# Kernel tuning notes

Hardware: AMD Instinct MI355X
Metric: run time of the kernel (lower is better)

Reference implementation:

```python
import jax, jax.numpy as jnp
import numpy as np

# Config (decoder-only Transformer)
NL, H, D, DK, V, B, S = 6, 16, 1024, 64, 32000, 2, 1024  # DK = d_v = D // H
DFF = 4 * D


def _layer_norm(x, g, b, eps=1e-5):
    mu = jnp.mean(x, axis=-1, keepdims=True)
    var = jnp.mean(jnp.square(x - mu), axis=-1, keepdims=True)
    return (x - mu) * jax.lax.rsqrt(var + eps) * g + b


def _pos_encoding(seq_len, d_embed):
    # Matches PositionalEncoding: base 1000 (as in source), sin at even i, cos at odd i
    pos = jnp.arange(seq_len, dtype=jnp.float32)[:, None]
    i = jnp.arange(d_embed, dtype=jnp.float32)[None, :]
    angle = pos / jnp.power(1000.0, i / d_embed)
    return jnp.where((jnp.arange(d_embed)[None, :] % 2) == 0, jnp.sin(angle), jnp.cos(angle))


def setup_inputs() -> dict:
    key = jax.random.key(0)
    ks = jax.random.split(key, 8)
    n = lambda k, shp, sc: jax.random.normal(k, shp, dtype=jnp.float32) * sc
    return {
        "outputs": jax.random.randint(ks[0], (B, S), 0, V),
        "embed": n(ks[1], (V, D), 0.02),
        # per-head Q/K/V projections stacked over layers and heads: [NL, H, D, DK]
        "Wq": n(ks[2], (NL, H, D, DK), D ** -0.5),
        "Wk": n(ks[3], (NL, H, D, DK), D ** -0.5),
        "Wv": n(ks[4], (NL, H, D, DK), D ** -0.5),
        "W1": n(ks[5], (NL, D, DFF), D ** -0.5),
        "W2": n(ks[6], (NL, DFF, D), DFF ** -0.5),
        "ln1_g": jnp.ones((NL, D), jnp.float32),
        "ln1_b": jnp.zeros((NL, D), jnp.float32),
        "ln2_g": jnp.ones((NL, D), jnp.float32),
        "ln2_b": jnp.zeros((NL, D), jnp.float32),
        "Wout": n(ks[7], (D, V), D ** -0.5),
        "bout": jnp.zeros((V,), jnp.float32),
    }


def reference(outputs, embed, Wq, Wk, Wv, W1, W2, ln1_g, ln1_b, ln2_g, ln2_b, Wout, bout):
    x = embed[outputs]                      # [B, S, D]
    x = x + _pos_encoding(S, D)
    scale = jnp.float32(DK ** 0.5)
    for l in range(NL):
        # Masked multi-head self-attention (per-head projections batched over H)
        q = jnp.einsum('bsd,hdk->bhsk', x, Wq[l])
        k = jnp.einsum('bsd,hdk->bhsk', x, Wk[l])
        v = jnp.einsum('bsd,hdk->bhsk', x, Wv[l])
        scores = jnp.einsum('bhqk,bhsk->bhqs', q, k) / scale   # [B,H,S,S]
        # Faithful to source: tril then masked_fill(score == 0, -inf)
        scores = jnp.tril(scores)
        scores = jnp.where(scores == 0, -jnp.inf, scores)
        w = jax.nn.softmax(scores, axis=-1)
        attn = jnp.einsum('bhqs,bhsv->bqhv', w, v).reshape(B, S, H * DK)
        x = _layer_norm(x + attn, ln1_g[l], ln1_b[l])
        # Position-wise FFN (dropout is identity at inference)
        h = jax.nn.relu(x @ W1[l]) @ W2[l]
        x = _layer_norm(x + h, ln2_g[l], ln2_b[l])
    return x @ Wout + bout                  # logits [B, S, V]
```

## Files before the change

kernel.cpp:

```cpp
#include <hip/hip_runtime.h>

typedef unsigned short u16;
typedef __attribute__((ext_vector_type(8))) short short8;
typedef __attribute__((ext_vector_type(4))) short short4_t;
typedef __attribute__((ext_vector_type(4))) float f32x4;

#define NLAYER 6
#define NH 16
#define DMODEL 1024
#define DHEAD 64
#define NVOCAB 32000
#define NB 2
#define NS 1024
#define NDFF 4096
#define MTOK (NB*NS)

__device__ __forceinline__ u16 f2b(float f) {
    union { float f; unsigned u; } x; x.f = f;
    unsigned r = x.u + 0x7fffu + ((x.u >> 16) & 1u);
    return (u16)(r >> 16);
}

#define GLL16(gp, lp) __builtin_amdgcn_global_load_lds( \
    (const __attribute__((address_space(1))) void*)(gp), \
    (__attribute__((address_space(3))) void*)(lp), 16, 0, 0)

__global__ __launch_bounds__(256) void trans64(
    const float* __restrict__ src, u16* __restrict__ dst,
    int R, int C, long sStride, long dStride)
{
    __shared__ float sh[64][65];
    const int c0 = blockIdx.x * 64, r0 = blockIdx.y * 64;
    const float* s = src + (long)blockIdx.z * sStride;
    u16* d = dst + (long)blockIdx.z * dStride;
    const int tid = threadIdx.x;
    const int lr = tid >> 4, lc = (tid & 15) * 4;
    #pragma unroll
    for (int q = 0; q < 4; ++q) {
        const float4 v = *(const float4*)(s + (long)(r0 + q * 16 + lr) * C + c0 + lc);
        sh[q * 16 + lr][lc + 0] = v.x;
        sh[q * 16 + lr][lc + 1] = v.y;
        sh[q * 16 + lr][lc + 2] = v.z;
        sh[q * 16 + lr][lc + 3] = v.w;
    }
    __syncthreads();
    #pragma unroll
    for (int k = 0; k < 2; ++k) {
        const int t = tid + 256 * k;
        const int col = t >> 3, rch = (t & 7) * 8;
        u16 tmp[8];
        #pragma unroll
        for (int j = 0; j < 8; ++j) tmp[j] = f2b(sh[rch + j][col]);
        *(short8*)(d + (long)(c0 + col) * R + r0 + rch) = *(const short8*)tmp;
    }
}

__global__ void transpose_qkv(const float* __restrict__ src, u16* __restrict__ dst, int sel)
{
    __shared__ float t[32][33];
    const int bi = blockIdx.z, l = bi >> 4, h = bi & 15;
    const float* s = src + (long)bi * (DMODEL * DHEAD);
    u16* d = dst + (long)l * 3072 * DMODEL + (long)(sel * 1024 + h * 64) * DMODEL;
    const int c0 = blockIdx.x * 32, r0 = blockIdx.y * 32;
    const int tx = threadIdx.x, ty = threadIdx.y;
    #pragma unroll
    for (int j = 0; j < 32; j += 8)
        t[ty + j][tx] = s[(long)(r0 + ty + j) * DHEAD + c0 + tx];
    __syncthreads();
    #pragma unroll
    for (int j = 0; j < 32; j += 8)
        d[(long)(c0 + ty + j) * DMODEL + r0 + tx] = f2b(t[tx][ty + j]);
}

__global__ void embed_pe(const int* __restrict__ toks, const float* __restrict__ emb,
                         float* __restrict__ x, u16* __restrict__ xb)
{
    const int row = blockIdx.x;
    const int s = row & (NS - 1);
    const long erow = (long)toks[row] * DMODEL;
    const long base = (long)row * DMODEL;
    #pragma unroll
    for (int j = 0; j < 4; ++j) {
        int d = threadIdx.x + j * 256;
        float ang = (float)s * exp2f(-(float)d * (9.965784284662087f / 1024.f));
        float pe = (d & 1) ? cosf(ang) : sinf(ang);
        float v = emb[erow + d] + pe;
        x[base + d] = v;
        xb[base + d] = f2b(v);
    }
}

template<int ND>
__global__ __launch_bounds__(256) void ln_residual(
    const float* __restrict__ xin, const float* __restrict__ delta, size_t pstride,
    const float* __restrict__ g, const float* __restrict__ bb,
    float* __restrict__ xout, u16* __restrict__ xbout)
{
    __shared__ float red[8];
    const long base = (long)blockIdx.x * DMODEL;
    const int d = threadIdx.x * 4;
    f32x4 v = *(const f32x4*)(xin + base + d);
    #pragma unroll
    for (int y = 0; y < ND; ++y)
        v += *(const f32x4*)(delta + base + (size_t)y * pstride + d);
    float sum = v[0] + v[1] + v[2] + v[3];
    float sq  = v[0]*v[0] + v[1]*v[1] + v[2]*v[2] + v[3]*v[3];
    #pragma unroll
    for (int off = 1; off < 64; off <<= 1) {
        sum += __shfl_xor(sum, off, 64);
        sq  += __shfl_xor(sq,  off, 64);
    }
    const int wv = threadIdx.x >> 6, lane = threadIdx.x & 63;
    if (lane == 0) { red[wv] = sum; red[4 + wv] = sq; }
    __syncthreads();
    float ts = red[0] + red[1] + red[2] + red[3];
    float tq = red[4] + red[5] + red[6] + red[7];
    float mu = ts * (1.f / DMODEL);
    float var = tq * (1.f / DMODEL) - mu * mu;
    float rstd = rsqrtf(var + 1e-5f);
    const f32x4 gg = *(const f32x4*)(g + d);
    const f32x4 bv = *(const f32x4*)(bb + d);
    f32x4 yv = (v - mu) * rstd * gg + bv;
    *(f32x4*)(xout + base + d) = yv;
    u16 fourv[4];
    #pragma unroll
    for (int i = 0; i < 4; ++i) fourv[i] = f2b(yv[i]);
    *(short4_t*)(xbout + base + d) = *(const short4_t*)fourv;
}

template<int BM, int EPI>
__global__ __launch_bounds__(BM*2, 2) void gemm_pipe(
    const u16* __restrict__ A, const u16* __restrict__ Bt,
    void* __restrict__ Cout, const float* __restrict__ bias,
    int M, int N, int K, int lda, int ldb, size_t zstride)
{
    constexpr int WAVES = BM / 32;
    constexpr int WC = WAVES / 2;
    constexpr int MR = BM / 32;
    constexpr int TILE = BM * 32;

    __shared__ __align__(16) u16 As[4][TILE];
    __shared__ __align__(16) u16 Bs[4][TILE];

    const int nmb = M / BM;
    const int id = blockIdx.x, nwg = gridDim.x;
    const int q = nwg >> 3, r = nwg & 7, xcd = id & 7, loc = id >> 3;
    const int swz = (xcd < r ? xcd * (q + 1) : r * (q + 1) + (xcd - r) * q) + loc;
    const int m0 = (swz % nmb) * BM, n0 = (swz / nmb) * BM;
    const int koff = blockIdx.y * K;

    const int tid = threadIdx.x, wv = tid >> 6, lane = tid & 63;
    const int wr = wv / WC, wc = wv % WC;
    const int lrow = lane & 15, ks = lane >> 4;

    const u16* gsrc[4];
    int ldso[2];
    {
        const int l4 = lane >> 2, s = lane & 3;
        #pragma unroll
        for (int j = 0; j < 2; ++j) {
            const int row = j * (WAVES * 16) + wv * 16 + l4;
            const int x = (row >> 1) & 3;
            gsrc[j]     = A  + (size_t)(m0 + row) * lda + koff + (size_t)((s ^ x) * 8);
            gsrc[2 + j] = Bt + (size_t)(n0 + row) * ldb + koff + (size_t)((s ^ x) * 8);
            ldso[j] = (j * (WAVES * 16) + wv * 16) * 32;
        }
    }
    int aoff[MR], boff[4];
    #pragma unroll
    for (int m = 0; m < MR; ++m) {
        const int row = wr * (BM / 2) + m * 16 + lrow;
        aoff[m] = row * 32 + ((ks ^ ((row >> 1) & 3)) * 8);
    }
    #pragma unroll
    for (int n = 0; n < 4; ++n) {
        const int row = wc * 64 + n * 16 + lrow;
        boff[n] = row * 32 + ((ks ^ ((row >> 1) & 3)) * 8);
    }

    const int NT = K / 32;
    auto ISSUE = [&](int t) {
        const int b = t & 3;
        const size_t ko = (size_t)t * 32;
        #pragma unroll
        for (int j = 0; j < 2; ++j) {
            GLL16(gsrc[j] + ko,     &As[b][ldso[j]]);
            GLL16(gsrc[2 + j] + ko, &Bs[b][ldso[j]]);
        }
    };

    f32x4 acc[MR][4] = {};
    ISSUE(0); ISSUE(1); ISSUE(2);

    for (int t = 0; t < NT; ++t) {
        if (t < NT - 2)       { asm volatile("s_waitcnt vmcnt(8)" ::: "memory"); }
        else if (t == NT - 2) { asm volatile("s_waitcnt vmcnt(4)" ::: "memory"); }
        else                  { asm volatile("s_waitcnt vmcnt(0)" ::: "memory"); }
        __builtin_amdgcn_sched_barrier(0);
        __builtin_amdgcn_s_barrier();
        __builtin_amdgcn_sched_barrier(0);

        const int b = t & 3;
        short8 af[MR], bf[4];
        #pragma unroll
        for (int m = 0; m < MR; ++m) af[m] = *(const short8*)(&As[b][aoff[m]]);
        #pragma unroll
        for (int n = 0; n < 4; ++n)  bf[n] = *(const short8*)(&Bs[b][boff[n]]);
        if (t + 3 < NT) ISSUE(t + 3);
        __builtin_amdgcn_s_setprio(1);
        #pragma unroll
        for (int m = 0; m < MR; ++m)
            #pragma unroll
            for (int n = 0; n < 4; ++n)
                acc[m][n] = __builtin_amdgcn_mfma_f32_16x16x32_bf16(af[m], bf[n], acc[m][n], 0, 0, 0);
        __builtin_amdgcn_s_setprio(0);
    }

    if (EPI == 0 || EPI == 3) {
        __syncthreads();
        float* patch = (float*)((WAVES == 8 && (wv & 4)) ? (void*)&Bs[0][0] : (void*)&As[0][0])
                       + (wv & 3) * (16 * 68);
        const int cc0 = n0 + wc * 64;
        f32x4 bvv = {};
        if (EPI == 3) bvv = *(const f32x4*)(bias + cc0 + (lane & 15) * 4);
        float* C = (float*)Cout + (EPI == 0 ? (size_t)blockIdx.y * zstride : (size_t)0);
        #pragma unroll
        for (int m = 0; m < MR; ++m) {
            #pragma unroll
            for (int n = 0; n < 4; ++n)
                #pragma unroll
                for (int i = 0; i < 4; ++i)
                    patch[(ks * 4 + i) * 68 + n * 16 + lrow] = acc[m][n][i];
            #pragma unroll
            for (int i2 = 0; i2 < 4; ++i2) {
                const int prow = i2 * 4 + ks;
                f32x4 v = *(const f32x4*)(patch + prow * 68 + (lane & 15) * 4);
                if (EPI == 3) v += bvv;
                const int rr = m0 + wr * (BM / 2) + m * 16 + prow;
                *(f32x4*)(C + (size_t)rr * N + cc0 + (lane & 15) * 4) = v;
            }
        }
    } else {
        u16* C = (u16*)Cout;
        #pragma unroll
        for (int m = 0; m < MR; ++m) {
            const int rr = m0 + wr * (BM / 2) + m * 16 + ks * 4;
            #pragma unroll
            for (int n = 0; n < 4; ++n) {
                const int cc = n0 + wc * 64 + n * 16 + lrow;
                #pragma unroll
                for (int i = 0; i < 4; ++i) {
                    float vv = acc[m][n][i];
                    if (EPI == 2) vv = fmaxf(vv, 0.f);
                    C[(size_t)(rr + i) * N + cc] = f2b(vv);
                }
            }
        }
    }
}

__global__ __launch_bounds__(256, 2) void attn_flash4(
    const u16* __restrict__ qk, const u16* __restrict__ vT, float* __restrict__ delta)
{
    __shared__ __align__(16) u16 Qs[64 * 64];
    __shared__ __align__(16) u16 Kd[2][64 * 64];
    __shared__ __align__(16) u16 Vd[2][64 * 64];
    __shared__ __align__(16) u16 Ps[4][16 * 64];

    const int pair = blockIdx.x, h = blockIdx.y, b = blockIdx.z;
    const int tid = threadIdx.x, wv = tid >> 6, lane = tid & 63;
    const int lrow = lane & 15, ks4 = lane >> 4, li4 = ks4 * 4;
    const long baseQK = (long)b * NS * 2048;
    const u16* vbase = vT + (long)h * 64 * 2048 + b * NS;
    u16* ps = &Ps[wv][0];

    for (int rep = 0; rep < 2; ++rep) {
        const int qt = rep ? 15 - pair : pair;
        __syncthreads();

        #pragma unroll
        for (int i = 0; i < 2; ++i) {
            const int c = (wv * 2 + i) * 64 + lane;
            const int row = c >> 3, u = (c & 7) ^ (row & 7);
            GLL16(qk + baseQK + (long)(qt * 64 + row) * 2048 + h * 64 + u * 8, Qs + c * 8);
            GLL16(qk + baseQK + (long)row * 2048 + 1024 + h * 64 + u * 8, Kd[0] + c * 8);
            GLL16(vbase + (long)row * 2048 + u * 8, Vd[0] + c * 8);
        }
        __syncthreads();

        short8 aq[2];
        {
            const int row = wv * 16 + lrow;
            aq[0] = *(const short8*)(Qs + row * 64 + ((ks4 ^ (row & 7)) * 8));
            aq[1] = *(const short8*)(Qs + row * 64 + (((4 + ks4) ^ (row & 7)) * 8));
        }

        f32x4 o[4] = {};
        float m_ = -__builtin_inff(), l_ = 0.f;

        for (int t = 0; t <= qt; ++t) {
            const int p = t & 1;
            if (t < qt) {
                #pragma unroll
                for (int i = 0; i < 2; ++i) {
                    const int c = (wv * 2 + i) * 64 + lane;
                    const int row = c >> 3, u = (c & 7) ^ (row & 7);
                    GLL16(qk + baseQK + (long)((t + 1) * 64 + row) * 2048 + 1024 + h * 64 + u * 8, Kd[p ^ 1] + c * 8);
                    GLL16(vbase + (long)row * 2048 + (t + 1) * 64 + u * 8, Vd[p ^ 1] + c * 8);
                }
            }
            f32x4 sa[4];
            #pragma unroll
            for (int nb = 0; nb < 4; ++nb) {
                f32x4 z = {};
                #pragma unroll
                for (int kd = 0; kd < 2; ++kd) {
                    const int row = nb * 16 + lrow;
                    short8 bk = *(const short8*)(Kd[p] + row * 64 + (((kd * 4 + ks4) ^ (row & 7)) * 8));
                    z = __builtin_amdgcn_mfma_f32_16x16x32_bf16(bk, aq[kd], z, 0, 0, 0);
                }
                sa[nb] = z;
            }
            const int qg = qt * 64 + wv * 16 + lrow;
            #pragma unroll
            for (int nb = 0; nb < 4; ++nb)
                #pragma unroll
                for (int i = 0; i < 4; ++i) {
                    float sc = sa[nb][i] * 0.125f;
                    if (t == qt && (t * 64 + nb * 16 + li4 + i) > qg) sc = -__builtin_inff();
                    sa[nb][i] = sc;
                }
            float mt = sa[0][0];
            #pragma unroll
            for (int nb = 0; nb < 4; ++nb)
                #pragma unroll
                for (int i = 0; i < 4; ++i) mt = fmaxf(mt, sa[nb][i]);
            mt = fmaxf(mt, __shfl_xor(mt, 16, 64));
            mt = fmaxf(mt, __shfl_xor(mt, 32, 64));
            const float mn = fmaxf(m_, mt);
            const float fac = expf(m_ - mn);
            m_ = mn;
            float rs = 0.f;
            #pragma unroll
            for (int nb = 0; nb < 4; ++nb)
                #pragma unroll
                for (int i = 0; i < 4; ++i) {
                    float pp = expf(sa[nb][i] - mn);
                    sa[nb][i] = pp; rs += pp;
                }
            rs += __shfl_xor(rs, 16, 64);
            rs += __shfl_xor(rs, 32, 64);
            l_ = l_ * fac + rs;
            #pragma unroll
            for (int nd = 0; nd < 4; ++nd) o[nd] *= fac;

            #pragma unroll
            for (int nb = 0; nb < 4; ++nb) {
                u16 fourv[4];
                #pragma unroll
                for (int i = 0; i < 4; ++i) fourv[i] = f2b(sa[nb][i]);
                const int kvb = nb * 16 + li4;
                const int addr = lrow * 64 + (((kvb >> 3) ^ (lrow & 7)) * 8) + (kvb & 7);
                *(short4_t*)(ps + addr) = *(const short4_t*)fourv;
            }
            short8 pa[2];
            pa[0] = *(const short8*)(ps + lrow * 64 + ((ks4 ^ (lrow & 7)) * 8));
            pa[1] = *(const short8*)(ps + lrow * 64 + (((4 + ks4) ^ (lrow & 7)) * 8));
            #pragma unroll
            for (int nd = 0; nd < 4; ++nd)
                #pragma unroll
                for (int kd = 0; kd < 2; ++kd) {
                    const int row = nd * 16 + lrow;
                    short8 vb = *(const short8*)(Vd[p] + row * 64 + (((kd * 4 + ks4) ^ (row & 7)) * 8));
                    o[nd] = __builtin_amdgcn_mfma_f32_16x16x32_bf16(vb, pa[kd], o[nd], 0, 0, 0);
                }
            __syncthreads();
        }

        const float inv = 1.f / l_;
        const long tok = (long)b * NS + qt * 64 + wv * 16 + lrow;
        #pragma unroll
        for (int nd = 0; nd < 4; ++nd) {
            f32x4 v = o[nd] * inv;
            *(f32x4*)(delta + tok * DMODEL + h * 64 + nd * 16 + li4) = v;
        }
    }
}

extern "C" void kernel_launch(void* const* d_in, const int* in_sizes, int n_in,
                              void* d_out, int out_size, void* d_ws, size_t ws_size,
                              hipStream_t stream) {
    const int*   toks  = (const int*)d_in[0];
    const float* emb   = (const float*)d_in[1];
    const float* Wq    = (const float*)d_in[2];
    const float* Wk    = (const float*)d_in[3];
    const float* Wv    = (const float*)d_in[4];
    const float* W1    = (const float*)d_in[5];
    const float* W2    = (const float*)d_in[6];
    const float* ln1g  = (const float*)d_in[7];
    const float* ln1b  = (const float*)d_in[8];
    const float* ln2g  = (const float*)d_in[9];
    const float* ln2b  = (const float*)d_in[10];
    const float* Wout  = (const float*)d_in[11];
    const float* bout  = (const float*)d_in[12];

    char* p = (char*)d_ws;
    auto alloc = [&](size_t bytes) { void* r = (void*)p; p += (bytes + 255) & ~(size_t)255; return r; };
    const size_t PSZ = (size_t)MTOK * 1024;
    u16*   Wqkv_t = (u16*)alloc((size_t)NLAYER * 3072 * 1024 * 2);
    u16*   W1t    = (u16*)alloc((size_t)NLAYER * 4096 * 1024 * 2);
    u16*   W2t    = (u16*)alloc((size_t)NLAYER * 1024 * 4096 * 2);
    u16*   Woutt  = (u16*)alloc((size_t)NVOCAB * 1024 * 2);
    float* x      = (float*)alloc((size_t)MTOK * 1024 * 4);
    u16*   xb     = (u16*)alloc((size_t)MTOK * 1024 * 2);
    u16*   qkbuf  = (u16*)alloc((size_t)MTOK * 2048 * 2);
    u16*   vTbuf  = (u16*)alloc((size_t)1024 * MTOK * 2);
    u16*   hbuf   = (u16*)alloc((size_t)MTOK * 4096 * 2);
    float* dbuf   = (float*)alloc(PSZ * 4 * 4);

    float* hbufF = (float*)hbuf;

    transpose_qkv<<<dim3(2, 32, 96), dim3(32, 8), 0, stream>>>(Wq, Wqkv_t, 0);
    transpose_qkv<<<dim3(2, 32, 96), dim3(32, 8), 0, stream>>>(Wk, Wqkv_t, 1);
    transpose_qkv<<<dim3(2, 32, 96), dim3(32, 8), 0, stream>>>(Wv, Wqkv_t, 2);
    trans64<<<dim3(64, 16, 6), 256, 0, stream>>>(W1, W1t, 1024, 4096, 1024l * 4096, 4096l * 1024);
    trans64<<<dim3(16, 64, 6), 256, 0, stream>>>(W2, W2t, 4096, 1024, 4096l * 1024, 1024l * 4096);
    trans64<<<dim3(500, 16, 1), 256, 0, stream>>>(Wout, Woutt, 1024, NVOCAB, 0, 0);

    embed_pe<<<MTOK, 256, 0, stream>>>(toks, emb, x, xb);

    for (int l = 0; l < NLAYER; ++l) {
        const u16* Wl = Wqkv_t + (size_t)l * 3072 * 1024;
        gemm_pipe<128, 1><<<dim3(16 * 16), 256, 0, stream>>>(
            xb, Wl, qkbuf, nullptr, MTOK, 2048, 1024, 1024, 1024, 0);
        gemm_pipe<128, 1><<<dim3(8 * 16), 256, 0, stream>>>(
            Wl + (size_t)2048 * 1024, xb, vTbuf, nullptr, 1024, MTOK, 1024, 1024, 1024, 0);
        attn_flash4<<<dim3(8, NH, NB), 256, 0, stream>>>(qkbuf, vTbuf, hbufF);
        ln_residual<1><<<MTOK, 256, 0, stream>>>(x, hbufF, 0,
            ln1g + l * 1024, ln1b + l * 1024, x, xb);
        gemm_pipe<128, 2><<<dim3(16 * 32), 256, 0, stream>>>(
            xb, W1t + (size_t)l * 4096 * 1024, hbuf, nullptr, MTOK, 4096, 1024, 1024, 1024, 0);
        gemm_pipe<128, 0><<<dim3(16 * 8, 4), 256, 0, stream>>>(
            hbuf, W2t + (size_t)l * 1024 * 4096, dbuf, nullptr, MTOK, 1024, 1024, 4096, 4096, PSZ);
        ln_residual<4><<<MTOK, 256, 0, stream>>>(x, dbuf, PSZ,
            ln2g + l * 1024, ln2b + l * 1024, x, xb);
    }

    gemm_pipe<256, 3><<<dim3(8 * 125), 512, 0, stream>>>(
        xb, Woutt, (float*)d_out, bout, MTOK, NVOCAB, 1024, 1024, 1024, 0);
}
```

Before: 1.158 ms.

## Merge QKV GEMMs, halve W2 split-K, add dedicated vocab GEMM kernel

Refactors the GEMM into a device body so the Q/K and V-transpose projections run in one combined 384-block launch. The W2 GEMM split-K factor drops from 4 to 2, which halves the partial-sum buffer and the reduction work in the following layernorm, at the cost of fewer blocks. The final vocabulary projection gets a new 128x256-tile, 256-thread kernel with double buffering and an extra barrier per k-step, replacing the 256x256 kernel. These changes aim to cut launch count, reduction traffic, and improve occupancy of the largest GEMM.

```diff
diff --git a/kernel.cpp b/kernel.cpp
--- a/kernel.cpp
+++ b/kernel.cpp
@@ -129,25 +129,22 @@
 }
 
 template<int BM, int EPI>
-__global__ __launch_bounds__(BM*2, 2) void gemm_pipe(
+__device__ __forceinline__ void gemm_body(
     const u16* __restrict__ A, const u16* __restrict__ Bt,
     void* __restrict__ Cout, const float* __restrict__ bias,
-    int M, int N, int K, int lda, int ldb, size_t zstride)
+    int M, int N, int K, int lda, int ldb, size_t zstride,
+    int id, int nwg, int zidx, u16* Asp, u16* Bsp)
 {
     constexpr int WAVES = BM / 32;
     constexpr int WC = WAVES / 2;
     constexpr int MR = BM / 32;
     constexpr int TILE = BM * 32;
 
-    __shared__ __align__(16) u16 As[4][TILE];
-    __shared__ __align__(16) u16 Bs[4][TILE];
-
     const int nmb = M / BM;
-    const int id = blockIdx.x, nwg = gridDim.x;
     const int q = nwg >> 3, r = nwg & 7, xcd = id & 7, loc = id >> 3;
     const int swz = (xcd < r ? xcd * (q + 1) : r * (q + 1) + (xcd - r) * q) + loc;
     const int m0 = (swz % nmb) * BM, n0 = (swz / nmb) * BM;
-    const int koff = blockIdx.y * K;
+    const int koff = zidx * K;
 
     const int tid = threadIdx.x, wv = tid >> 6, lane = tid & 63;
     const int wr = wv / WC, wc = wv % WC;
@@ -184,8 +181,8 @@
         const size_t ko = (size_t)t * 32;
         #pragma unroll
         for (int j = 0; j < 2; ++j) {
-            GLL16(gsrc[j] + ko,     &As[b][ldso[j]]);
-            GLL16(gsrc[2 + j] + ko, &Bs[b][ldso[j]]);
+            GLL16(gsrc[j] + ko,     Asp + b * TILE + ldso[j]);
+            GLL16(gsrc[2 + j] + ko, Bsp + b * TILE + ldso[j]);
         }
     };
 
@@ -203,9 +200,9 @@
         const int b = t & 3;
         short8 af[MR], bf[4];
         #pragma unroll
-        for (int m = 0; m < MR; ++m) af[m] = *(const short8*)(&As[b][aoff[m]]);
-        #pragma unroll
-        for (int n = 0; n < 4; ++n)  bf[n] = *(const short8*)(&Bs[b][boff[n]]);
+        for (int m = 0; m < MR; ++m) af[m] = *(const short8*)(Asp + b * TILE + aoff[m]);
+        #pragma unroll
+        for (int n = 0; n < 4; ++n)  bf[n] = *(const short8*)(Bsp + b * TILE + boff[n]);
         if (t + 3 < NT) ISSUE(t + 3);
         __builtin_amdgcn_s_setprio(1);
         #pragma unroll
@@ -218,12 +215,12 @@
 
     if (EPI == 0 || EPI == 3) {
         __syncthreads();
-        float* patch = (float*)((WAVES == 8 && (wv & 4)) ? (void*)&Bs[0][0] : (void*)&As[0][0])
+        float* patch = (float*)((WAVES == 8 && (wv & 4)) ? (void*)Bsp : (void*)Asp)
                        + (wv & 3) * (16 * 68);
         const int cc0 = n0 + wc * 64;
         f32x4 bvv = {};
         if (EPI == 3) bvv = *(const f32x4*)(bias + cc0 + (lane & 15) * 4);
-        float* C = (float*)Cout + (EPI == 0 ? (size_t)blockIdx.y * zstride : (size_t)0);
+        float* C = (float*)Cout + (EPI == 0 ? (size_t)zidx * zstride : (size_t)0);
         #pragma unroll
         for (int m = 0; m < MR; ++m) {
             #pragma unroll
@@ -255,6 +252,139 @@
                     C[(size_t)(rr + i) * N + cc] = f2b(vv);
                 }
             }
+        }
+    }
+}
+
+template<int BM, int EPI>
+__global__ __launch_bounds__(BM*2, 2) void gemm_pipe(
+    const u16* __restrict__ A, const u16* __restrict__ Bt,
+    void* __restrict__ Cout, const float* __restrict__ bias,
+    int M, int N, int K, int lda, int ldb, size_t zstride)
+{
+    __shared__ __align__(16) u16 As[4][BM * 32];
+    __shared__ __align__(16) u16 Bs[4][BM * 32];
+    gemm_body<BM, EPI>(A, Bt, Cout, bias, M, N, K, lda, ldb, zstride,
+                       blockIdx.x, gridDim.x, blockIdx.y, &As[0][0], &Bs[0][0]);
+}
+
+__global__ __launch_bounds__(256, 2) void gemm_qkv(
+    const u16* __restrict__ xb, const u16* __restrict__ Wl,
+    u16* __restrict__ qkbuf, u16* __restrict__ vTbuf)
+{
+    __shared__ __align__(16) u16 As[4][128 * 32];
+    __shared__ __align__(16) u16 Bs[4][128 * 32];
+    if (blockIdx.x < 256)
+        gemm_body<128, 1>(xb, Wl, qkbuf, nullptr, MTOK, 2048, 1024, 1024, 1024, 0,
+                          blockIdx.x, 256, 0, &As[0][0], &Bs[0][0]);
+    else
+        gemm_body<128, 1>(Wl + (size_t)2048 * 1024, xb, vTbuf, nullptr, 1024, MTOK, 1024,
+                          1024, 1024, 0, blockIdx.x - 256, 128, 0, &As[0][0], &Bs[0][0]);
+}
+
+__global__ __launch_bounds__(256, 2) void gemm_voc(
+    const u16* __restrict__ A, const u16* __restrict__ Bt,
+    float* __restrict__ C, const float* __restrict__ bias,
+    int M, int N, int K)
+{
+    __shared__ __align__(16) u16 As[2][128 * 32];
+    __shared__ __align__(16) u16 Bs[2][256 * 32];
+
+    const int nmb = M >> 7;
+    const int id = blockIdx.x, nwg = gridDim.x;
+    const int q = nwg >> 3, r = nwg & 7, xcd = id & 7, loc = id >> 3;
+    const int swz = (xcd < r ? xcd * (q + 1) : r * (q + 1) + (xcd - r) * q) + loc;
+    const int m0 = (swz % nmb) * 128, n0 = (swz / nmb) * 256;
+
+    const int tid = threadIdx.x, wv = tid >> 6, lane = tid & 63;
+    const int wr = wv >> 1, wc = wv & 1;
+    const int lrow = lane & 15, ks = lane >> 4;
+
+    const u16* srcA[2]; int dsoA[2];
+    const u16* srcB[4]; int dsoB[4];
+    #pragma unroll
+    for (int i = 0; i < 2; ++i) {
+        const int c = tid + i * 256, row = c >> 2, s = c & 3;
+        srcA[i] = A + (size_t)(m0 + row) * K + (size_t)(((s ^ ((row >> 1) & 3))) * 8);
+        dsoA[i] = c * 8;
+    }
+    #pragma unroll
+    for (int i = 0; i < 4; ++i) {
+        const int c = tid + i * 256, row = c >> 2, s = c & 3;
+        srcB[i] = Bt + (size_t)(n0 + row) * K + (size_t)(((s ^ ((row >> 1) & 3))) * 8);
+        dsoB[i] = c * 8;
+    }
+    int aoff[4], boff[8];
+    #pragma unroll
+    for (int m = 0; m < 4; ++m) {
+        const int row = wr * 64 + m * 16 + lrow;
+        aoff[m] = row * 32 + ((ks ^ ((row >> 1) & 3)) * 8);
+    }
+    #pragma unroll
+    for (int n = 0; n < 8; ++n) {
+        const int row = wc * 128 + n * 16 + lrow;
+        boff[n] = row * 32 + ((ks ^ ((row >> 1) & 3)) * 8);
+    }
+
+    const int NT = K >> 5;
+    auto ISSUE = [&](int t) {
+        const int b = t & 1;
+        const size_t ko = (size_t)t * 32;
+        #pragma unroll
+        for (int i = 0; i < 2; ++i) GLL16(srcA[i] + ko, &As[b][dsoA[i]]);
+        #pragma unroll
+        for (int i = 0; i < 4; ++i) GLL16(srcB[i] + ko, &Bs[b][dsoB[i]]);
+    };
+
+    f32x4 acc[4][8] = {};
+    ISSUE(0); ISSUE(1);
+
+    for (int t = 0; t < NT; ++t) {
+        if (t < NT - 1) { asm volatile("s_waitcnt vmcnt(6)" ::: "memory"); }
+        else            { asm volatile("s_waitcnt vmcnt(0)" ::: "memory"); }
+        __builtin_amdgcn_sched_barrier(0);
+        __builtin_amdgcn_s_barrier();
+        __builtin_amdgcn_sched_barrier(0);
+
+        const int b = t & 1;
+        short8 af[4], bf[8];
+        #pragma unroll
+        for (int m = 0; m < 4; ++m) af[m] = *(const short8*)(&As[b][aoff[m]]);
+        #pragma unroll
+        for (int n = 0; n < 8; ++n) bf[n] = *(const short8*)(&Bs[b][boff[n]]);
+        asm volatile("s_waitcnt lgkmcnt(0)" ::: "memory");
+        __builtin_amdgcn_sched_barrier(0);
+        __builtin_amdgcn_s_barrier();
+        __builtin_amdgcn_sched_barrier(0);
+        if (t + 2 < NT) ISSUE(t + 2);
+        __builtin_amdgcn_s_setprio(1);
+        #pragma unroll
+        for (int m = 0; m < 4; ++m)
+            #pragma unroll
+            for (int n = 0; n < 8; ++n)
+                acc[m][n] = __builtin_amdgcn_mfma_f32_16x16x32_bf16(af[m], bf[n], acc[m][n], 0, 0, 0);
+        __builtin_amdgcn_s_setprio(0);
+    }
+
+    __syncthreads();
+    float* patch = (wv == 0) ? (float*)&As[0][0]
+                             : (float*)&Bs[0][0] + (wv - 1) * (16 * 136);
+    const int cc0 = n0 + wc * 128;
+    const int l32 = lane & 31, lh = lane >> 5;
+    const f32x4 bvv = *(const f32x4*)(bias + cc0 + l32 * 4);
+    #pragma unroll
+    for (int m = 0; m < 4; ++m) {
+        #pragma unroll
+        for (int n = 0; n < 8; ++n)
+            #pragma unroll
+            for (int i = 0; i < 4; ++i)
+                patch[(ks * 4 + i) * 136 + n * 16 + lrow] = acc[m][n][i];
+        #pragma unroll
+        for (int j = 0; j < 8; ++j) {
+            const int prow = j * 2 + lh;
+            f32x4 v = *(const f32x4*)(patch + prow * 136 + l32 * 4) + bvv;
+            const int rr = m0 + wr * 64 + m * 16 + prow;
+            *(f32x4*)(C + (size_t)rr * N + cc0 + l32 * 4) = v;
         }
     }
 }
@@ -416,7 +546,7 @@
     u16*   qkbuf  = (u16*)alloc((size_t)MTOK * 2048 * 2);
     u16*   vTbuf  = (u16*)alloc((size_t)1024 * MTOK * 2);
     u16*   hbuf   = (u16*)alloc((size_t)MTOK * 4096 * 2);
-    float* dbuf   = (float*)alloc(PSZ * 4 * 4);
+    float* dbuf   = (float*)alloc(PSZ * 2 * 4);
 
     float* hbufF = (float*)hbuf;
 
@@ -431,21 +561,18 @@
 
     for (int l = 0; l < NLAYER; ++l) {
         const u16* Wl = Wqkv_t + (size_t)l * 3072 * 1024;
-        gemm_pipe<128, 1><<<dim3(16 * 16), 256, 0, stream>>>(
-            xb, Wl, qkbuf, nullptr, MTOK, 2048, 1024, 1024, 1024, 0);
-        gemm_pipe<128, 1><<<dim3(8 * 16), 256, 0, stream>>>(
-            Wl + (size_t)2048 * 1024, xb, vTbuf, nullptr, 1024, MTOK, 1024, 1024, 1024, 0);
+        gemm_qkv<<<dim3(384), 256, 0, stream>>>(xb, Wl, qkbuf, vTbuf);
         attn_flash4<<<dim3(8, NH, NB), 256, 0, stream>>>(qkbuf, vTbuf, hbufF);
         ln_residual<1><<<MTOK, 256, 0, stream>>>(x, hbufF, 0,
             ln1g + l * 1024, ln1b + l * 1024, x, xb);
         gemm_pipe<128, 2><<<dim3(16 * 32), 256, 0, stream>>>(
             xb, W1t + (size_t)l * 4096 * 1024, hbuf, nullptr, MTOK, 4096, 1024, 1024, 1024, 0);
-        gemm_pipe<128, 0><<<dim3(16 * 8, 4), 256, 0, stream>>>(
-            hbuf, W2t + (size_t)l * 1024 * 4096, dbuf, nullptr, MTOK, 1024, 1024, 4096, 4096, PSZ);
-        ln_residual<4><<<MTOK, 256, 0, stream>>>(x, dbuf, PSZ,
+        gemm_pipe<128, 0><<<dim3(16 * 8, 2), 256, 0, stream>>>(
+            hbuf, W2t + (size_t)l * 1024 * 4096, dbuf, nullptr, MTOK, 1024, 2048, 4096, 4096, PSZ);
+        ln_residual<2><<<MTOK, 256, 0, stream>>>(x, dbuf, PSZ,
             ln2g + l * 1024, ln2b + l * 1024, x, xb);
     }
 
-    gemm_pipe<256, 3><<<dim3(8 * 125), 512, 0, stream>>>(
-        xb, Woutt, (float*)d_out, bout, MTOK, NVOCAB, 1024, 1024, 1024, 0);
-}
+    gemm_voc<<<dim3(16 * 125), 256, 0, stream>>>(
+        xb, Woutt, (float*)d_out, bout, MTOK, NVOCAB, 1024);
+}
```

Result: faster. 1.115 ms (-3.7%).
